# Performance work log

Hardware: AMD Instinct MI355X
Metric: run time of the kernel (lower is better)

## Reference

```python
import jax, jax.numpy as jnp
import numpy as np

B, C, H, W = 64, 64, 56, 56
MID = 2 * C  # two output nodes concatenated
EPS = 1e-5


def _conv1x1(x, w):
    # x: [B,C,H,W], w: [O,C] (1x1 conv kernel squeezed)
    return jnp.einsum('bchw,oc->bohw', x, w)


def _bn(x, g, b, m, v):
    # eval-mode BatchNorm2d with running stats
    sc = g * jax.lax.rsqrt(v + EPS)
    return x * sc[None, :, None, None] + (b - m * sc)[None, :, None, None]


def _maxpool3(x):
    # MaxPool2d(kernel=3, stride=1, padding=1)
    return jax.lax.reduce_window(x, -jnp.inf, jax.lax.max,
                                 (1, 1, 3, 3), (1, 1, 1, 1),
                                 [(0, 0), (0, 0), (1, 1), (1, 1)])


def _avgpool3(x):
    # AvgPool2d(kernel=3, stride=1, padding=1), count_include_pad=True -> /9
    s = jax.lax.reduce_window(x, 0.0, jax.lax.add,
                              (1, 1, 3, 3), (1, 1, 1, 1),
                              [(0, 0), (0, 0), (1, 1), (1, 1)])
    return s * (1.0 / 9.0)


def setup_inputs() -> dict:
    key = jax.random.key(0)
    ks = jax.random.split(key, 11)
    x = jax.random.normal(ks[0], (B, C, H, W), dtype=jnp.float32)
    w1 = jax.random.normal(ks[1], (C, C), dtype=jnp.float32) * 0.1
    w2 = jax.random.normal(ks[2], (C, MID), dtype=jnp.float32) * 0.1
    bn1_g = 1.0 + 0.1 * jax.random.normal(ks[3], (C,), dtype=jnp.float32)
    bn1_b = 0.1 * jax.random.normal(ks[4], (C,), dtype=jnp.float32)
    bn1_m = 0.1 * jax.random.normal(ks[5], (C,), dtype=jnp.float32)
    bn1_v = jax.random.uniform(ks[6], (C,), minval=0.5, maxval=1.5, dtype=jnp.float32)
    bn2_g = 1.0 + 0.1 * jax.random.normal(ks[7], (C,), dtype=jnp.float32)
    bn2_b = 0.1 * jax.random.normal(ks[8], (C,), dtype=jnp.float32)
    bn2_m = 0.1 * jax.random.normal(ks[9], (C,), dtype=jnp.float32)
    bn2_v = jax.random.uniform(ks[10], (C,), minval=0.5, maxval=1.5, dtype=jnp.float32)
    return dict(x=x, w1=w1, w2=w2,
                bn1_g=bn1_g, bn1_b=bn1_b, bn1_m=bn1_m, bn1_v=bn1_v,
                bn2_g=bn2_g, bn2_b=bn2_b, bn2_m=bn2_m, bn2_v=bn2_v)


def reference(x, w1, w2, bn1_g, bn1_b, bn1_m, bn1_v, bn2_g, bn2_b, bn2_m, bn2_v):
    # DAG g = [[[0,1],[1,2]], [[4,3],[3]], [[5,3],[3,100]], [[4,3],[100]]]
    # topoSort order: [0, 2, 1, 3]; output nodes (ordered): [2, 3]
    node0 = jax.nn.relu(_bn(_conv1x1(x, w1), bn1_g, bn1_b, bn1_m, bn1_v))
    node1 = _maxpool3(node0)            # op type 4, pred {0}
    node2 = _avgpool3(node0)            # op type 5, pred {0}
    node3 = _maxpool3(node1) + _maxpool3(node2)  # op type 4, preds {1,2}, summed
    cat = jnp.concatenate([node2, node3], axis=1)  # [B, 2C, H, W]
    out = jax.nn.relu(_bn(_conv1x1(cat, w2), bn2_g, bn2_b, bn2_m, bn2_v))
    return out
```

## Files before the change

### kernel.cpp

```cpp
#include <hip/hip_runtime.h>
#include <cstddef>

#define EPS 1e-5f
static constexpr int Bn = 64, Cn = 64, Hn = 56, Wn = 56, HWn = Hn * Wn;
static constexpr int XS = 65;
static constexpr int RB = 8;
static constexpr int NBAND = 7;
static constexpr int BPX = RB * Wn;
static constexpr int SLAB = 3600;

typedef __attribute__((ext_vector_type(8))) short short8;
typedef __attribute__((ext_vector_type(8))) unsigned short ushort8;
typedef __attribute__((ext_vector_type(4))) float floatx4;
typedef __attribute__((ext_vector_type(16))) float floatx16;
typedef __attribute__((ext_vector_type(4))) unsigned int uintx4;
typedef __attribute__((ext_vector_type(2))) unsigned int uintx2;

__device__ __forceinline__ unsigned pack_rne(float a, float b) {
    unsigned ua = __float_as_uint(a), ub = __float_as_uint(b);
    ua = ua + 0x7fffu + ((ua >> 16) & 1u);
    ub = ub + 0x7fffu + ((ub >> 16) & 1u);
    return __builtin_amdgcn_perm(ub, ua, 0x07060302);
}
__device__ __forceinline__ unsigned pack_trunc(float a, float b) {
    return __builtin_amdgcn_perm(__float_as_uint(b), __float_as_uint(a), 0x07060302);
}
__device__ __forceinline__ ushort8 pmax(ushort8 a, ushort8 b) {
    return __builtin_elementwise_max(a, b);
}
__device__ __forceinline__ float bf_lo(unsigned u) { return __uint_as_float(u << 16); }
__device__ __forceinline__ float bf_hi(unsigned u) { return __uint_as_float(u & 0xffff0000u); }


__global__ __launch_bounds__(256) void k1_conv1(
    const float* __restrict__ x, const float* __restrict__ w1,
    const float* __restrict__ bg, const float* __restrict__ bb,
    const float* __restrict__ bm, const float* __restrict__ bv,
    unsigned short* __restrict__ node0)
{
    __shared__ float xs[2][64 * XS];
    __shared__ float scs[64], shs[64];
    const int tid = threadIdx.x;
    if (tid < 64) {
        float sc = bg[tid] * rsqrtf(bv[tid] + EPS);
        scs[tid] = sc;
        shs[tid] = bb[tid] - bm[tid] * sc;
    }
    __syncthreads();
    const int lane = tid & 63;
    const int wv   = tid >> 6;
    const int m    = lane & 15;
    const int quad = lane >> 4;
    const int qoff = quad * 8;

    short8 afr[4][2];
    float shv[16];
    #pragma unroll
    for (int t = 0; t < 4; ++t) {
        const float sc = scs[t * 16 + m];
        #pragma unroll
        for (int kk = 0; kk < 2; ++kk) {
            const float* wp = w1 + (t * 16 + m) * 64 + kk * 32 + qoff;
            floatx4 f0 = *(const floatx4*)wp;
            floatx4 f1 = *(const floatx4*)(wp + 4);
            uintx4 u;
            u.x = pack_rne(f0[0] * sc, f0[1] * sc);
            u.y = pack_rne(f0[2] * sc, f0[3] * sc);
            u.z = pack_rne(f1[0] * sc, f1[1] * sc);
            u.w = pack_rne(f1[2] * sc, f1[3] * sc);
            afr[t][kk] = *(short8*)&u;
        }
        #pragma unroll
        for (int i = 0; i < 4; ++i) shv[t * 4 + i] = shs[t * 16 + quad * 4 + i];
    }

    floatx4 stg[4];
    auto ldtile = [&](int tt) {
        const int P = blockIdx.x * 256 + tt * 64;
        const int b = P / HWn, p0 = P - b * HWn;
        #pragma unroll
        for (int q = 0; q < 4; ++q) {
            int idx = q * 256 + tid;
            int c = idx >> 4, f = idx & 15;
            stg[q] = *(const floatx4*)(x + (size_t)(b * 64 + c) * HWn + p0 + f * 4);
        }
    };
    auto sttile = [&](int buf) {
        #pragma unroll
        for (int q = 0; q < 4; ++q) {
            int idx = q * 256 + tid;
            int c = idx >> 4, f = idx & 15;
            #pragma unroll
            for (int k = 0; k < 4; ++k)
                xs[buf][(f * 4 + k) * XS + c] = stg[q][k];
        }
    };

    ldtile(0);
    sttile(0);

    #pragma unroll
    for (int tt = 0; tt < 4; ++tt) {
        __syncthreads();
        if (tt < 3) ldtile(tt + 1);

        const int P = blockIdx.x * 256 + tt * 64;
        const int b = P / HWn, p0 = P - b * HWn;
        const float* xr = &xs[tt & 1][(wv * 16 + m) * XS];

        floatx4 acc[4];
        #pragma unroll
        for (int t = 0; t < 4; ++t) acc[t] = (floatx4){0.f, 0.f, 0.f, 0.f};

        #pragma unroll
        for (int kk = 0; kk < 2; ++kk) {
            float f[8];
            #pragma unroll
            for (int j = 0; j < 8; ++j) f[j] = xr[kk * 32 + qoff + j];
            uintx4 u;
            u.x = pack_trunc(f[0], f[1]);
            u.y = pack_trunc(f[2], f[3]);
            u.z = pack_trunc(f[4], f[5]);
            u.w = pack_trunc(f[6], f[7]);
            short8 bfr = *(short8*)&u;
            #pragma unroll
            for (int t = 0; t < 4; ++t)
                acc[t] = __builtin_amdgcn_mfma_f32_16x16x32_bf16(afr[t][kk], bfr, acc[t], 0, 0, 0);
        }

        const int chunkbase = (quad >> 1);
        const int j0 = (quad & 1) * 4;
        #pragma unroll
        for (int t = 0; t < 4; ++t) {
            float v0 = acc[t][0] + shv[t * 4 + 0]; v0 = v0 > 0.f ? v0 : 0.f;
            float v1 = acc[t][1] + shv[t * 4 + 1]; v1 = v1 > 0.f ? v1 : 0.f;
            float v2 = acc[t][2] + shv[t * 4 + 2]; v2 = v2 > 0.f ? v2 : 0.f;
            float v3 = acc[t][3] + shv[t * 4 + 3]; v3 = v3 > 0.f ? v3 : 0.f;
            uintx2 st;
            st.x = pack_rne(v0, v1);
            st.y = pack_rne(v2, v3);
            int chunk = t * 2 + chunkbase;
            *(uintx2*)(node0 + ((size_t)(b * 8 + chunk) * HWn + p0 + wv * 16 + m) * 8 + j0) = st;
        }

        if (tt < 3) sttile((tt + 1) & 1);
    }
}

__global__ __launch_bounds__(512) void k23_fused(
    const unsigned short* __restrict__ node0,
    const float* __restrict__ w2,
    const float* __restrict__ bg, const float* __restrict__ bb,
    const float* __restrict__ bm, const float* __restrict__ bv,
    float* __restrict__ out)
{
    __shared__ __align__(16) unsigned short catl[16 * SLAB];
    const int tid = threadIdx.x;
    const int lane = tid & 63;
    const int wv = tid >> 6;

    int bid = blockIdx.x;
    bid = (bid & 7) * 56 + (bid >> 3);
    const int band = bid % NBAND;
    const int b = bid / NBAND;
    const int lo = band * RB;

    const int m = lane & 15;
    const int q = lane >> 4;
    const int t = wv >> 1;

    short8 afr[4];
    #pragma unroll
    for (int cp = 0; cp < 4; ++cp) {
        const int c = 2 * cp + (q >> 1);
        const int chb = ((q & 1) ? 64 : 0) + 8 * c;
        const float* wp = w2 + (size_t)(t * 16 + m) * 128 + chb;
        floatx4 f0 = *(const floatx4*)wp;
        floatx4 f1 = *(const floatx4*)(wp + 4);
        uintx4 u;
        u.x = pack_rne(f0[0], f0[1]);
        u.y = pack_rne(f0[2], f0[3]);
        u.z = pack_rne(f1[0], f1[1]);
        u.w = pack_rne(f1[2], f1[3]);
        afr[cp] = *(short8*)&u;
    }
    const int oc0 = t * 16 + q * 4;
    floatx4 g4 = *(const floatx4*)(bg + oc0);
    floatx4 bb4 = *(const floatx4*)(bb + oc0);
    floatx4 mm4 = *(const floatx4*)(bm + oc0);
    floatx4 vv4 = *(const floatx4*)(bv + oc0);
    float sc[4], sh[4];
    #pragma unroll
    for (int r = 0; r < 4; ++r) {
        sc[r] = g4[r] * rsqrtf(vv4[r] + EPS);
        sh[r] = bb4[r] - mm4[r] * sc[r];
    }

    {
        const int chunk = wv;
        const int col = lane;
        const bool act = col < Wn;
        const unsigned short* base = node0 + ((size_t)(b * 8 + chunk) * HWn) * 8;
        unsigned short* cav = catl + (size_t)(chunk * 2 + 0) * SLAB;
        unsigned short* cmx = catl + (size_t)(chunk * 2 + 1) * SLAB;

        const ushort8 zz = (ushort8)0;
        auto load5 = [&](int r, ushort8* d) {
            #pragma unroll
            for (int dd = 0; dd < 5; ++dd) {
                int cc = col + dd - 2;
                bool ok = act && ((unsigned)cc < (unsigned)Wn) && ((unsigned)r < (unsigned)Hn);
                d[dd] = ok ? *(const ushort8*)(base + (size_t)(r * Wn + cc) * 8) : zz;
            }
        };

        float hs1[8], hs2[8];
        ushort8 h5a = zz, h5b = zz, h5c = zz, h5d = zz, nh1 = zz, nh2 = zz;
        #pragma unroll
        for (int j = 0; j < 8; ++j) hs1[j] = hs2[j] = 0.f;

        ushort8 d[5];
        load5(lo - 2, d);

        #pragma unroll
        for (int i = 0; i < 12; ++i) {
            const int r = lo - 2 + i;
            ushort8 dn[5];
            if (i < 11) load5(r + 1, dn);

            ushort8 hm5 = pmax(pmax(pmax(d[0], d[1]), pmax(d[2], d[3])), d[4]);
            ushort8 m5 = pmax(pmax(pmax(h5a, h5b), pmax(h5c, h5d)), hm5);
            h5a = h5b; h5b = h5c; h5c = h5d; h5d = hm5;

            const uintx4 ul = *(const uintx4*)&d[1];
            const uintx4 uv = *(const uintx4*)&d[2];
            const uintx4 ur = *(const uintx4*)&d[3];
            float a2[8];
            const int r2 = r - 1, r3 = r - 2;
            const bool v2 = (unsigned)r2 < (unsigned)Hn;
            #pragma unroll
            for (int w = 0; w < 4; ++w) {
                float hsum0 = bf_lo(ul[w]) + bf_lo(uv[w]) + bf_lo(ur[w]);
                float hsum1 = bf_hi(ul[w]) + bf_hi(uv[w]) + bf_hi(ur[w]);
                a2[w * 2 + 0] = v2 ? (hs2[w * 2 + 0] + hs1[w * 2 + 0] + hsum0) * (1.f / 9.f) : 0.f;
                a2[w * 2 + 1] = v2 ? (hs2[w * 2 + 1] + hs1[w * 2 + 1] + hsum1) * (1.f / 9.f) : 0.f;
                hs2[w * 2 + 0] = hs1[w * 2 + 0]; hs1[w * 2 + 0] = hsum0;
                hs2[w * 2 + 1] = hs1[w * 2 + 1]; hs1[w * 2 + 1] = hsum1;
            }
            uintx4 ap;
            ap.x = pack_rne(a2[0], a2[1]);
            ap.y = pack_rne(a2[2], a2[3]);
            ap.z = pack_rne(a2[4], a2[5]);
            ap.w = pack_rne(a2[6], a2[7]);
            uintx4 al, ar;
            #pragma unroll
            for (int w = 0; w < 4; ++w) {
                unsigned u = ap[w];
                unsigned lu = __shfl_up(u, 1);
                unsigned ru = __shfl_down(u, 1);
                al[w] = (lane == 0) ? 0u : lu;
                ar[w] = (lane == 63) ? 0u : ru;
            }
            ushort8 nh = pmax(pmax(*(ushort8*)&al, *(ushort8*)&ap), *(ushort8*)&ar);
            ushort8 m3 = pmax(pmax(nh2, nh1), nh);
            nh2 = nh1; nh1 = nh;

            if (act && r2 >= lo && r2 < lo + RB)
                *(uintx4*)(cav + (size_t)((r2 - lo) * Wn + col) * 8) = ap;
            if (act && r3 >= lo && r3 < lo + RB) {
                const uintx4 u5 = *(const uintx4*)&m5;
                const uintx4 u3 = *(const uintx4*)&m3;
                uintx4 st;
                #pragma unroll
                for (int w = 0; w < 4; ++w)
                    st[w] = pack_rne(bf_lo(u5[w]) + bf_lo(u3[w]), bf_hi(u5[w]) + bf_hi(u3[w]));
                *(uintx4*)(cmx + (size_t)((r3 - lo) * Wn + col) * 8) = st;
            }
            #pragma unroll
            for (int dd = 0; dd < 5; ++dd) d[dd] = dn[dd];
        }
    }
    __syncthreads();

    floatx4 acc[14];
    #pragma unroll
    for (int i = 0; i < 14; ++i) acc[i] = (floatx4){0.f, 0.f, 0.f, 0.f};

    #pragma unroll
    for (int cp = 0; cp < 4; ++cp) {
        #pragma unroll
        for (int i = 0; i < 14; ++i) {
            const int px = ((wv & 1) * 14 + i) * 16 + m;
            short8 bfr = *(const short8*)(catl + (size_t)(4 * cp + q) * SLAB + (size_t)px * 8);
            acc[i] = __builtin_amdgcn_mfma_f32_16x16x32_bf16(afr[cp], bfr, acc[i], 0, 0, 0);
        }
    }

    float* ob = out + (size_t)(b * 64 + oc0) * HWn + lo * Wn;
    #pragma unroll
    for (int i = 0; i < 14; ++i) {
        const int px = ((wv & 1) * 14 + i) * 16 + m;
        #pragma unroll
        for (int r = 0; r < 4; ++r) {
            float v = fmaf(acc[i][r], sc[r], sh[r]);
            ob[(size_t)r * HWn + px] = v > 0.f ? v : 0.f;
        }
    }
}

extern "C" void kernel_launch(void* const* d_in, const int* in_sizes, int n_in,
                              void* d_out, int out_size, void* d_ws, size_t ws_size,
                              hipStream_t stream)
{
    const float* x   = (const float*)d_in[0];
    const float* w1  = (const float*)d_in[1];
    const float* w2  = (const float*)d_in[2];
    const float* b1g = (const float*)d_in[3];
    const float* b1b = (const float*)d_in[4];
    const float* b1m = (const float*)d_in[5];
    const float* b1v = (const float*)d_in[6];
    const float* b2g = (const float*)d_in[7];
    const float* b2b = (const float*)d_in[8];
    const float* b2m = (const float*)d_in[9];
    const float* b2v = (const float*)d_in[10];

    float* out = (float*)d_out;
    unsigned short* node0 = (unsigned short*)d_ws;

    k1_conv1<<<dim3(784), dim3(256), 0, stream>>>(x, w1, b1g, b1b, b1m, b1v, node0);
    k23_fused<<<dim3(Bn * NBAND), dim3(512), 0, stream>>>(node0, w2, b2g, b2b, b2m, b2v, out);
}
```

Before: 153.0 us.

## Halve row band size, load one column per lane and shuffle neighbors

Cuts the fused pool+conv kernel's row band from 8 to 4 rows, doubling the grid to 896 blocks and halving the LDS slab so up to 4 blocks fit per CU (launch_bounds 512,4). Each lane now loads only its own column per row and gets left/right neighbours via wave shuffles instead of five overlapping global loads. The w2/BN parameter loads move after the pooling phase to shorten register live ranges. The smaller band raises halo overhead (8 rows read for 4 output rows versus 12 for 8) in exchange for more occupancy and fewer redundant loads.

```diff
diff --git a/kernel.cpp b/kernel.cpp
--- a/kernel.cpp
+++ b/kernel.cpp
@@ -4,10 +4,10 @@
 #define EPS 1e-5f
 static constexpr int Bn = 64, Cn = 64, Hn = 56, Wn = 56, HWn = Hn * Wn;
 static constexpr int XS = 65;
-static constexpr int RB = 8;
-static constexpr int NBAND = 7;
+static constexpr int RB = 4;
+static constexpr int NBAND = 14;
 static constexpr int BPX = RB * Wn;
-static constexpr int SLAB = 3600;
+static constexpr int SLAB = 1808;
 
 typedef __attribute__((ext_vector_type(8))) short short8;
 typedef __attribute__((ext_vector_type(8))) unsigned short ushort8;
@@ -147,7 +147,7 @@
     }
 }
 
-__global__ __launch_bounds__(512) void k23_fused(
+__global__ __launch_bounds__(512, 4) void k23_fused(
     const unsigned short* __restrict__ node0,
     const float* __restrict__ w2,
     const float* __restrict__ bg, const float* __restrict__ bb,
@@ -160,7 +160,7 @@
     const int wv = tid >> 6;
 
     int bid = blockIdx.x;
-    bid = (bid & 7) * 56 + (bid >> 3);
+    bid = (bid & 7) * 112 + (bid >> 3);
     const int band = bid % NBAND;
     const int b = bid / NBAND;
     const int lo = band * RB;
@@ -168,33 +168,6 @@
     const int m = lane & 15;
     const int q = lane >> 4;
     const int t = wv >> 1;
-
-    short8 afr[4];
-    #pragma unroll
-    for (int cp = 0; cp < 4; ++cp) {
-        const int c = 2 * cp + (q >> 1);
-        const int chb = ((q & 1) ? 64 : 0) + 8 * c;
-        const float* wp = w2 + (size_t)(t * 16 + m) * 128 + chb;
-        floatx4 f0 = *(const floatx4*)wp;
-        floatx4 f1 = *(const floatx4*)(wp + 4);
-        uintx4 u;
-        u.x = pack_rne(f0[0], f0[1]);
-        u.y = pack_rne(f0[2], f0[3]);
-        u.z = pack_rne(f1[0], f1[1]);
-        u.w = pack_rne(f1[2], f1[3]);
-        afr[cp] = *(short8*)&u;
-    }
-    const int oc0 = t * 16 + q * 4;
-    floatx4 g4 = *(const floatx4*)(bg + oc0);
-    floatx4 bb4 = *(const floatx4*)(bb + oc0);
-    floatx4 mm4 = *(const floatx4*)(bm + oc0);
-    floatx4 vv4 = *(const floatx4*)(bv + oc0);
-    float sc[4], sh[4];
-    #pragma unroll
-    for (int r = 0; r < 4; ++r) {
-        sc[r] = g4[r] * rsqrtf(vv4[r] + EPS);
-        sh[r] = bb4[r] - mm4[r] * sc[r];
-    }
 
     {
         const int chunk = wv;
@@ -205,13 +178,9 @@
         unsigned short* cmx = catl + (size_t)(chunk * 2 + 1) * SLAB;
 
         const ushort8 zz = (ushort8)0;
-        auto load5 = [&](int r, ushort8* d) {
-            #pragma unroll
-            for (int dd = 0; dd < 5; ++dd) {
-                int cc = col + dd - 2;
-                bool ok = act && ((unsigned)cc < (unsigned)Wn) && ((unsigned)r < (unsigned)Hn);
-                d[dd] = ok ? *(const ushort8*)(base + (size_t)(r * Wn + cc) * 8) : zz;
-            }
+        auto loadrow = [&](int r) -> ushort8 {
+            bool ok = act && ((unsigned)r < (unsigned)Hn);
+            return ok ? *(const ushort8*)(base + (size_t)(r * Wn + col) * 8) : zz;
         };
 
         float hs1[8], hs2[8];
@@ -219,25 +188,43 @@
         #pragma unroll
         for (int j = 0; j < 8; ++j) hs1[j] = hs2[j] = 0.f;
 
-        ushort8 d[5];
-        load5(lo - 2, d);
-
-        #pragma unroll
-        for (int i = 0; i < 12; ++i) {
+        ushort8 cur = loadrow(lo - 2);
+
+        #pragma unroll
+        for (int i = 0; i < RB + 4; ++i) {
             const int r = lo - 2 + i;
-            ushort8 dn[5];
-            if (i < 11) load5(r + 1, dn);
-
-            ushort8 hm5 = pmax(pmax(pmax(d[0], d[1]), pmax(d[2], d[3])), d[4]);
+            ushort8 nxt = zz;
+            if (i < RB + 3) nxt = loadrow(r + 1);
+
+            const uintx4 uc = *(const uintx4*)&cur;
+            uintx4 t0, t1, t3, t4;
+            #pragma unroll
+            for (int w = 0; w < 4; ++w) {
+                unsigned u = uc[w];
+                unsigned l1 = __shfl_up(u, 1);
+                unsigned l2 = __shfl_up(u, 2);
+                unsigned r1 = __shfl_down(u, 1);
+                unsigned r2v = __shfl_down(u, 2);
+                t0[w] = (lane < 2) ? 0u : l2;
+                t1[w] = (lane < 1) ? 0u : l1;
+                t3[w] = r1;
+                t4[w] = r2v;
+            }
+            const ushort8 D0 = *(const ushort8*)&t0;
+            const ushort8 D1 = *(const ushort8*)&t1;
+            const ushort8 D3 = *(const ushort8*)&t3;
+            const ushort8 D4 = *(const ushort8*)&t4;
+
+            ushort8 hm5 = pmax(pmax(pmax(D0, D1), pmax(cur, D3)), D4);
             ushort8 m5 = pmax(pmax(pmax(h5a, h5b), pmax(h5c, h5d)), hm5);
             h5a = h5b; h5b = h5c; h5c = h5d; h5d = hm5;
 
-            const uintx4 ul = *(const uintx4*)&d[1];
-            const uintx4 uv = *(const uintx4*)&d[2];
-            const uintx4 ur = *(const uintx4*)&d[3];
+            const uintx4 ul = t1;
+            const uintx4 uv = uc;
+            const uintx4 ur = t3;
             float a2[8];
             const int r2 = r - 1, r3 = r - 2;
-            const bool v2 = (unsigned)r2 < (unsigned)Hn;
+            const bool v2 = ((unsigned)r2 < (unsigned)Hn) && act;
             #pragma unroll
             for (int w = 0; w < 4; ++w) {
                 float hsum0 = bf_lo(ul[w]) + bf_lo(uv[w]) + bf_lo(ur[w]);
@@ -276,21 +263,47 @@
                     st[w] = pack_rne(bf_lo(u5[w]) + bf_lo(u3[w]), bf_hi(u5[w]) + bf_hi(u3[w]));
                 *(uintx4*)(cmx + (size_t)((r3 - lo) * Wn + col) * 8) = st;
             }
-            #pragma unroll
-            for (int dd = 0; dd < 5; ++dd) d[dd] = dn[dd];
-        }
+            cur = nxt;
+        }
+    }
+
+    short8 afr[4];
+    #pragma unroll
+    for (int cp = 0; cp < 4; ++cp) {
+        const int c = 2 * cp + (q >> 1);
+        const int chb = ((q & 1) ? 64 : 0) + 8 * c;
+        const float* wp = w2 + (size_t)(t * 16 + m) * 128 + chb;
+        floatx4 f0 = *(const floatx4*)wp;
+        floatx4 f1 = *(const floatx4*)(wp + 4);
+        uintx4 u;
+        u.x = pack_rne(f0[0], f0[1]);
+        u.y = pack_rne(f0[2], f0[3]);
+        u.z = pack_rne(f1[0], f1[1]);
+        u.w = pack_rne(f1[2], f1[3]);
+        afr[cp] = *(short8*)&u;
+    }
+    const int oc0 = t * 16 + q * 4;
+    floatx4 g4 = *(const floatx4*)(bg + oc0);
+    floatx4 bb4 = *(const floatx4*)(bb + oc0);
+    floatx4 mm4 = *(const floatx4*)(bm + oc0);
+    floatx4 vv4 = *(const floatx4*)(bv + oc0);
+    float sc[4], sh[4];
+    #pragma unroll
+    for (int r = 0; r < 4; ++r) {
+        sc[r] = g4[r] * rsqrtf(vv4[r] + EPS);
+        sh[r] = bb4[r] - mm4[r] * sc[r];
     }
     __syncthreads();
 
-    floatx4 acc[14];
-    #pragma unroll
-    for (int i = 0; i < 14; ++i) acc[i] = (floatx4){0.f, 0.f, 0.f, 0.f};
+    floatx4 acc[7];
+    #pragma unroll
+    for (int i = 0; i < 7; ++i) acc[i] = (floatx4){0.f, 0.f, 0.f, 0.f};
 
     #pragma unroll
     for (int cp = 0; cp < 4; ++cp) {
         #pragma unroll
-        for (int i = 0; i < 14; ++i) {
-            const int px = ((wv & 1) * 14 + i) * 16 + m;
+        for (int i = 0; i < 7; ++i) {
+            const int px = ((wv & 1) * 7 + i) * 16 + m;
             short8 bfr = *(const short8*)(catl + (size_t)(4 * cp + q) * SLAB + (size_t)px * 8);
             acc[i] = __builtin_amdgcn_mfma_f32_16x16x32_bf16(afr[cp], bfr, acc[i], 0, 0, 0);
         }
@@ -298,8 +311,8 @@
 
     float* ob = out + (size_t)(b * 64 + oc0) * HWn + lo * Wn;
     #pragma unroll
-    for (int i = 0; i < 14; ++i) {
-        const int px = ((wv & 1) * 14 + i) * 16 + m;
+    for (int i = 0; i < 7; ++i) {
+        const int px = ((wv & 1) * 7 + i) * 16 + m;
         #pragma unroll
         for (int r = 0; r < 4; ++r) {
             float v = fmaf(acc[i][r], sc[r], sh[r]);
```

After: 156.0 us. About the same (+1.9%).

## Use 1024-thread blocks with shuffle-based neighbor loads in fused pool+conv kernel

Applied to the files above, without the earlier changes.

The fused pooling/conv2 kernel goes from 512 to 1024 threads. Each lane now handles half a channel chunk (4 bf16 values) for one column in a 28-column half-row, and horizontal neighbours come from wave shuffles instead of five redundant global loads per row. The MFMA stage is split so each wave computes 7 pixel tiles instead of 14, which cuts accumulator registers. The block-to-XCD mapping is also rewritten. This trades fewer redundant global loads and more threads per block for extra shuffle instructions and halo lanes that do no stores.

```diff
diff --git a/kernel.cpp b/kernel.cpp
--- a/kernel.cpp
+++ b/kernel.cpp
@@ -6,13 +6,12 @@
 static constexpr int XS = 65;
 static constexpr int RB = 8;
 static constexpr int NBAND = 7;
-static constexpr int BPX = RB * Wn;
 static constexpr int SLAB = 3600;
 
 typedef __attribute__((ext_vector_type(8))) short short8;
 typedef __attribute__((ext_vector_type(8))) unsigned short ushort8;
+typedef __attribute__((ext_vector_type(4))) unsigned short ushort4v;
 typedef __attribute__((ext_vector_type(4))) float floatx4;
-typedef __attribute__((ext_vector_type(16))) float floatx16;
 typedef __attribute__((ext_vector_type(4))) unsigned int uintx4;
 typedef __attribute__((ext_vector_type(2))) unsigned int uintx2;
 
@@ -27,6 +26,10 @@
 }
 __device__ __forceinline__ ushort8 pmax(ushort8 a, ushort8 b) {
     return __builtin_elementwise_max(a, b);
+}
+__device__ __forceinline__ uintx2 pmax2(uintx2 a, uintx2 b) {
+    ushort4v r = __builtin_elementwise_max(*(ushort4v*)&a, *(ushort4v*)&b);
+    return *(uintx2*)&r;
 }
 __device__ __forceinline__ float bf_lo(unsigned u) { return __uint_as_float(u << 16); }
 __device__ __forceinline__ float bf_hi(unsigned u) { return __uint_as_float(u & 0xffff0000u); }
@@ -147,7 +150,7 @@
     }
 }
 
-__global__ __launch_bounds__(512) void k23_fused(
+__global__ __launch_bounds__(1024, 4) void k23_fused(
     const unsigned short* __restrict__ node0,
     const float* __restrict__ w2,
     const float* __restrict__ bg, const float* __restrict__ bb,
@@ -159,22 +162,105 @@
     const int lane = tid & 63;
     const int wv = tid >> 6;
 
-    int bid = blockIdx.x;
-    bid = (bid & 7) * 56 + (bid >> 3);
-    const int band = bid % NBAND;
-    const int b = bid / NBAND;
+    const int bid = blockIdx.x;
+    const int xcd = bid & 7;
+    const int jj = bid >> 3;
+    const int b = xcd * 8 + jj / NBAND;
+    const int band = jj % NBAND;
     const int lo = band * RB;
 
-    const int m = lane & 15;
+    {
+        const int chunk = wv >> 1;
+        const int c0 = (wv & 1) * 28;
+        const int local = lane >> 1;
+        const int col = c0 - 2 + local;
+        const int jh = lane & 1;
+        const unsigned short* base = node0 + ((size_t)(b * 8 + chunk) * HWn) * 8 + jh * 4;
+
+        const uintx2 zz = (uintx2){0u, 0u};
+        auto loadrow = [&](int r) -> uintx2 {
+            if (((unsigned)col >= (unsigned)Wn) | ((unsigned)r >= (unsigned)Hn)) return zz;
+            return *(const uintx2*)(base + (size_t)(r * Wn + col) * 8);
+        };
+
+        float hs1[4], hs2[4];
+        #pragma unroll
+        for (int c = 0; c < 4; ++c) hs1[c] = hs2[c] = 0.f;
+        uintx2 h5a = zz, h5b = zz, h5c = zz, h5d = zz, nh1 = zz, nh2 = zz;
+
+        uintx2 cur = loadrow(lo - 2);
+        uintx2 nxt = loadrow(lo - 1);
+
+        unsigned short* cav = catl + (size_t)(chunk * 2) * SLAB + jh * 4;
+        unsigned short* cmx = cav + SLAB;
+        const bool stcol = (local >= 2) & (local <= 29);
+
+        #pragma unroll
+        for (int i = 0; i < RB + 4; ++i) {
+            const int r = lo - 2 + i;
+            uintx2 nx2 = (i < RB + 2) ? loadrow(r + 2) : zz;
+
+            uintx2 D0, D1, D3, D4;
+            #pragma unroll
+            for (int w = 0; w < 2; ++w) {
+                unsigned u = cur[w];
+                D1[w] = __shfl_up(u, 2);
+                D0[w] = __shfl_up(u, 4);
+                D3[w] = __shfl_down(u, 2);
+                D4[w] = __shfl_down(u, 4);
+            }
+
+            uintx2 hm5 = pmax2(pmax2(pmax2(D0, D1), pmax2(cur, D3)), D4);
+            uintx2 m5 = pmax2(pmax2(pmax2(h5a, h5b), pmax2(h5c, h5d)), hm5);
+            h5a = h5b; h5b = h5c; h5c = h5d; h5d = hm5;
+
+            float a2[4];
+            #pragma unroll
+            for (int w = 0; w < 2; ++w) {
+                float s0 = bf_lo(D1[w]) + bf_lo(cur[w]) + bf_lo(D3[w]);
+                float s1 = bf_hi(D1[w]) + bf_hi(cur[w]) + bf_hi(D3[w]);
+                a2[w * 2 + 0] = (hs2[w * 2 + 0] + hs1[w * 2 + 0] + s0) * (1.f / 9.f);
+                a2[w * 2 + 1] = (hs2[w * 2 + 1] + hs1[w * 2 + 1] + s1) * (1.f / 9.f);
+                hs2[w * 2 + 0] = hs1[w * 2 + 0]; hs1[w * 2 + 0] = s0;
+                hs2[w * 2 + 1] = hs1[w * 2 + 1]; hs1[w * 2 + 1] = s1;
+            }
+            uintx2 ap;
+            ap.x = pack_rne(a2[0], a2[1]);
+            ap.y = pack_rne(a2[2], a2[3]);
+
+            uintx2 al, ar;
+            #pragma unroll
+            for (int w = 0; w < 2; ++w) {
+                al[w] = __shfl_up(ap[w], 2);
+                ar[w] = __shfl_down(ap[w], 2);
+            }
+            uintx2 nh = pmax2(pmax2(al, ap), ar);
+            uintx2 m3 = pmax2(pmax2(nh2, nh1), nh);
+            nh2 = nh1; nh1 = nh;
+
+            const int r2 = r - 1, r3 = r - 2;
+            if (stcol && i >= 3 && i <= RB + 2)
+                *(uintx2*)(cav + (size_t)((r2 - lo) * Wn + col) * 8) = ap;
+            if (stcol && i >= 4) {
+                uintx2 st;
+                st.x = pack_rne(bf_lo(m5.x) + bf_lo(m3.x), bf_hi(m5.x) + bf_hi(m3.x));
+                st.y = pack_rne(bf_lo(m5.y) + bf_lo(m3.y), bf_hi(m5.y) + bf_hi(m3.y));
+                *(uintx2*)(cmx + (size_t)((r3 - lo) * Wn + col) * 8) = st;
+            }
+            cur = nxt; nxt = nx2;
+        }
+    }
+
+    const int m16 = lane & 15;
     const int q = lane >> 4;
-    const int t = wv >> 1;
-
+    const int t = wv & 3;
+    const int e = wv >> 2;
     short8 afr[4];
     #pragma unroll
     for (int cp = 0; cp < 4; ++cp) {
         const int c = 2 * cp + (q >> 1);
         const int chb = ((q & 1) ? 64 : 0) + 8 * c;
-        const float* wp = w2 + (size_t)(t * 16 + m) * 128 + chb;
+        const float* wp = w2 + (size_t)(t * 16 + m16) * 128 + chb;
         floatx4 f0 = *(const floatx4*)wp;
         floatx4 f1 = *(const floatx4*)(wp + 4);
         uintx4 u;
@@ -195,102 +281,17 @@
         sc[r] = g4[r] * rsqrtf(vv4[r] + EPS);
         sh[r] = bb4[r] - mm4[r] * sc[r];
     }
-
-    {
-        const int chunk = wv;
-        const int col = lane;
-        const bool act = col < Wn;
-        const unsigned short* base = node0 + ((size_t)(b * 8 + chunk) * HWn) * 8;
-        unsigned short* cav = catl + (size_t)(chunk * 2 + 0) * SLAB;
-        unsigned short* cmx = catl + (size_t)(chunk * 2 + 1) * SLAB;
-
-        const ushort8 zz = (ushort8)0;
-        auto load5 = [&](int r, ushort8* d) {
-            #pragma unroll
-            for (int dd = 0; dd < 5; ++dd) {
-                int cc = col + dd - 2;
-                bool ok = act && ((unsigned)cc < (unsigned)Wn) && ((unsigned)r < (unsigned)Hn);
-                d[dd] = ok ? *(const ushort8*)(base + (size_t)(r * Wn + cc) * 8) : zz;
-            }
-        };
-
-        float hs1[8], hs2[8];
-        ushort8 h5a = zz, h5b = zz, h5c = zz, h5d = zz, nh1 = zz, nh2 = zz;
-        #pragma unroll
-        for (int j = 0; j < 8; ++j) hs1[j] = hs2[j] = 0.f;
-
-        ushort8 d[5];
-        load5(lo - 2, d);
-
-        #pragma unroll
-        for (int i = 0; i < 12; ++i) {
-            const int r = lo - 2 + i;
-            ushort8 dn[5];
-            if (i < 11) load5(r + 1, dn);
-
-            ushort8 hm5 = pmax(pmax(pmax(d[0], d[1]), pmax(d[2], d[3])), d[4]);
-            ushort8 m5 = pmax(pmax(pmax(h5a, h5b), pmax(h5c, h5d)), hm5);
-            h5a = h5b; h5b = h5c; h5c = h5d; h5d = hm5;
-
-            const uintx4 ul = *(const uintx4*)&d[1];
-            const uintx4 uv = *(const uintx4*)&d[2];
-            const uintx4 ur = *(const uintx4*)&d[3];
-            float a2[8];
-            const int r2 = r - 1, r3 = r - 2;
-            const bool v2 = (unsigned)r2 < (unsigned)Hn;
-            #pragma unroll
-            for (int w = 0; w < 4; ++w) {
-                float hsum0 = bf_lo(ul[w]) + bf_lo(uv[w]) + bf_lo(ur[w]);
-                float hsum1 = bf_hi(ul[w]) + bf_hi(uv[w]) + bf_hi(ur[w]);
-                a2[w * 2 + 0] = v2 ? (hs2[w * 2 + 0] + hs1[w * 2 + 0] + hsum0) * (1.f / 9.f) : 0.f;
-                a2[w * 2 + 1] = v2 ? (hs2[w * 2 + 1] + hs1[w * 2 + 1] + hsum1) * (1.f / 9.f) : 0.f;
-                hs2[w * 2 + 0] = hs1[w * 2 + 0]; hs1[w * 2 + 0] = hsum0;
-                hs2[w * 2 + 1] = hs1[w * 2 + 1]; hs1[w * 2 + 1] = hsum1;
-            }
-            uintx4 ap;
-            ap.x = pack_rne(a2[0], a2[1]);
-            ap.y = pack_rne(a2[2], a2[3]);
-            ap.z = pack_rne(a2[4], a2[5]);
-            ap.w = pack_rne(a2[6], a2[7]);
-            uintx4 al, ar;
-            #pragma unroll
-            for (int w = 0; w < 4; ++w) {
-                unsigned u = ap[w];
-                unsigned lu = __shfl_up(u, 1);
-                unsigned ru = __shfl_down(u, 1);
-                al[w] = (lane == 0) ? 0u : lu;
-                ar[w] = (lane == 63) ? 0u : ru;
-            }
-            ushort8 nh = pmax(pmax(*(ushort8*)&al, *(ushort8*)&ap), *(ushort8*)&ar);
-            ushort8 m3 = pmax(pmax(nh2, nh1), nh);
-            nh2 = nh1; nh1 = nh;
-
-            if (act && r2 >= lo && r2 < lo + RB)
-                *(uintx4*)(cav + (size_t)((r2 - lo) * Wn + col) * 8) = ap;
-            if (act && r3 >= lo && r3 < lo + RB) {
-                const uintx4 u5 = *(const uintx4*)&m5;
-                const uintx4 u3 = *(const uintx4*)&m3;
-                uintx4 st;
-                #pragma unroll
-                for (int w = 0; w < 4; ++w)
-                    st[w] = pack_rne(bf_lo(u5[w]) + bf_lo(u3[w]), bf_hi(u5[w]) + bf_hi(u3[w]));
-                *(uintx4*)(cmx + (size_t)((r3 - lo) * Wn + col) * 8) = st;
-            }
-            #pragma unroll
-            for (int dd = 0; dd < 5; ++dd) d[dd] = dn[dd];
-        }
-    }
     __syncthreads();
 
-    floatx4 acc[14];
-    #pragma unroll
-    for (int i = 0; i < 14; ++i) acc[i] = (floatx4){0.f, 0.f, 0.f, 0.f};
+    floatx4 acc[7];
+    #pragma unroll
+    for (int i = 0; i < 7; ++i) acc[i] = (floatx4){0.f, 0.f, 0.f, 0.f};
 
     #pragma unroll
     for (int cp = 0; cp < 4; ++cp) {
         #pragma unroll
-        for (int i = 0; i < 14; ++i) {
-            const int px = ((wv & 1) * 14 + i) * 16 + m;
+        for (int i = 0; i < 7; ++i) {
+            const int px = (e * 7 + i) * 16 + m16;
             short8 bfr = *(const short8*)(catl + (size_t)(4 * cp + q) * SLAB + (size_t)px * 8);
             acc[i] = __builtin_amdgcn_mfma_f32_16x16x32_bf16(afr[cp], bfr, acc[i], 0, 0, 0);
         }
@@ -298,8 +299,8 @@
 
     float* ob = out + (size_t)(b * 64 + oc0) * HWn + lo * Wn;
     #pragma unroll
-    for (int i = 0; i < 14; ++i) {
-        const int px = ((wv & 1) * 14 + i) * 16 + m;
+    for (int i = 0; i < 7; ++i) {
+        const int px = (e * 7 + i) * 16 + m16;
         #pragma unroll
         for (int r = 0; r < 4; ++r) {
             float v = fmaf(acc[i][r], sc[r], sh[r]);
@@ -328,5 +329,5 @@
     unsigned short* node0 = (unsigned short*)d_ws;
 
     k1_conv1<<<dim3(784), dim3(256), 0, stream>>>(x, w1, b1g, b1b, b1m, b1v, node0);
-    k23_fused<<<dim3(Bn * NBAND), dim3(512), 0, stream>>>(node0, w2, b2g, b2b, b2m, b2v, out);
-}
+    k23_fused<<<dim3(Bn * NBAND), dim3(1024), 0, stream>>>(node0, w2, b2g, b2b, b2m, b2v, out);
+}
```

Result: faster. 146.6 us (-4.2%).
